# Performance work log

Hardware: AMD Instinct MI355X
Metric: run time of the kernel (lower is better)

## Reference

```python
import jax, jax.numpy as jnp
import numpy as np

WINDOW = (2, 7, 7)
NUM_HEADS = 8


def _relative_position_index(ws):
    d, h, w = ws
    coords = np.stack(np.meshgrid(np.arange(d), np.arange(h), np.arange(w), indexing='ij'), 0)
    cf = coords.reshape(3, -1)                      # [3, N]
    rel = (cf[:, :, None] - cf[:, None, :]).transpose(1, 2, 0)  # [N, N, 3]
    rel[..., 0] += d - 1
    rel[..., 1] += h - 1
    rel[..., 2] += w - 1
    idx = rel[..., 0] * ((2 * h - 1) * (2 * w - 1)) + rel[..., 1] * (2 * w - 1) + rel[..., 2]
    return idx.astype(np.int32)                     # [N, N]

_REL_IDX = _relative_position_index(WINDOW)


def setup_inputs() -> dict:
    key = jax.random.key(0)
    ks = jax.random.split(key, 6)
    B_, N, C = 2048, 98, 256
    nW = 64
    table_size = (2 * WINDOW[0] - 1) * (2 * WINDOW[1] - 1) * (2 * WINDOW[2] - 1)  # 507
    return {
        'x': jax.random.normal(ks[0], (B_, N, C), jnp.float32),
        'mask': jax.random.normal(ks[1], (nW, N, N), jnp.float32),
        'qkv_w': jax.random.normal(ks[2], (C, 3 * C), jnp.float32) * 0.02,
        'proj_w': jax.random.normal(ks[3], (C, C), jnp.float32) * 0.02,
        'proj_b': jax.random.normal(ks[4], (C,), jnp.float32) * 0.02,
        'bias_table': jax.random.normal(ks[5], (table_size, NUM_HEADS), jnp.float32) * 0.02,
    }


def reference(x, mask, qkv_w, proj_w, proj_b, bias_table):
    B_, N, C = x.shape
    H = NUM_HEADS
    Dh = C // H
    scale = Dh ** (-0.5)

    qkv = jnp.einsum('bnc,cd->bnd', x, qkv_w)               # [B_, N, 3C]
    qkv = qkv.reshape(B_, N, 3, H, Dh).transpose(2, 0, 3, 1, 4)  # [3, B_, H, N, Dh]
    q, k, v = qkv[0], qkv[1], qkv[2]

    attn = jnp.einsum('bhnd,bhmd->bhnm', q * scale, k)      # [B_, H, N, N]

    rel_idx = jnp.asarray(_REL_IDX[:N, :N])
    bias = bias_table[rel_idx.reshape(-1)].reshape(N, N, H).transpose(2, 0, 1)  # [H, N, N]
    attn = attn + bias[None]

    nW = mask.shape[0]
    attn = attn.reshape(B_ // nW, nW, H, N, N) + mask[None, :, None, :, :]
    attn = attn.reshape(B_, H, N, N)
    attn = jax.nn.softmax(attn, axis=-1)

    out = jnp.einsum('bhnm,bhmd->bhnd', attn, v)            # [B_, H, N, Dh]
    out = out.transpose(0, 2, 1, 3).reshape(B_, N, C)
    out = jnp.einsum('bnc,cd->bnd', out, proj_w) + proj_b
    return out
```

## Files before the change

### kernel.cpp

```cpp
#include <hip/hip_runtime.h>
#include <stdint.h>

typedef __bf16 bf16_t;
typedef __bf16 bf16x8 __attribute__((ext_vector_type(8)));
typedef float f32x4 __attribute__((ext_vector_type(4)));

#define MFMA16(a, b, c) __builtin_amdgcn_mfma_f32_16x16x32_bf16(a, b, c, 0, 0, 0)

__device__ __forceinline__ void gload_lds16(const bf16_t* g, bf16_t* l) {
  __builtin_amdgcn_global_load_lds(
      (const __attribute__((address_space(1))) void*)g,
      (__attribute__((address_space(3))) void*)l, 16, 0, 0);
}

__device__ __forceinline__ int sw4(int i) {
  return ((i & 3) << 2) | ((i >> 2) & 3);
}

__global__ __launch_bounds__(256) void cvt_x_k(const float* __restrict__ x,
                                               bf16_t* __restrict__ xb, int n8) {
  int i = blockIdx.x * 256 + threadIdx.x;
  if (i >= n8) return;
  const float4* xp = (const float4*)x + (size_t)i * 2;
  float4 f0 = xp[0], f1 = xp[1];
  bf16x8 o = {(bf16_t)f0.x, (bf16_t)f0.y, (bf16_t)f0.z, (bf16_t)f0.w,
              (bf16_t)f1.x, (bf16_t)f1.y, (bf16_t)f1.z, (bf16_t)f1.w};
  *(bf16x8*)(xb + (size_t)i * 8) = o;
}

__global__ __launch_bounds__(256) void cvt_wT_k(const float* __restrict__ w,
                                                bf16_t* __restrict__ wT, int N) {
  int n = blockIdx.x, k = threadIdx.x;
  wT[(size_t)n * 256 + k] = (bf16_t)w[(size_t)k * N + n];
}

__global__ __launch_bounds__(256) void gemm256(const bf16_t* __restrict__ A,
                                               const bf16_t* __restrict__ BT,
                                               int ncols,
                                               bf16_t* __restrict__ outb,
                                               float* __restrict__ outf,
                                               const float* __restrict__ bias) {
  __shared__ __align__(16) bf16_t sA[128 * 64];
  __shared__ __align__(16) bf16_t sB[128 * 64];
  const int tid = threadIdx.x;
  const int lane = tid & 63, wave = tid >> 6;
  const int lm = lane & 15, quad = lane >> 4;
  const int mBase = blockIdx.y * 128;
  const int nBase = blockIdx.x * 128;
  const int wm = (wave >> 1) * 64, wn = (wave & 1) * 64;

  f32x4 acc[4][4];
#pragma unroll
  for (int i = 0; i < 4; i++)
#pragma unroll
    for (int j = 0; j < 4; j++) acc[i][j] = {0.f, 0.f, 0.f, 0.f};

  const bf16_t* Ab = A + (size_t)mBase * 256;
  const bf16_t* Bb = BT + (size_t)nBase * 256;

  for (int kb = 0; kb < 4; ++kb) {
    const int k0 = kb * 64;
#pragma unroll
    for (int it = 0; it < 4; ++it) {
      int cid = it * 256 + wave * 64 + lane;
      int row = cid >> 3, kcp = cid & 7;
      int kcl = kcp ^ (row & 7);
      bf16_t* dstA = sA + (it * 256 + wave * 64) * 8;
      bf16_t* dstB = sB + (it * 256 + wave * 64) * 8;
      gload_lds16(Ab + (size_t)row * 256 + k0 + kcl * 8, dstA);
      gload_lds16(Bb + (size_t)row * 256 + k0 + kcl * 8, dstB);
    }
    __syncthreads();
#pragma unroll
    for (int kk = 0; kk < 64; kk += 32) {
      int c = (kk >> 3) + quad;
      bf16x8 af[4], bfr[4];
#pragma unroll
      for (int mt = 0; mt < 4; mt++) {
        int m = wm + mt * 16 + lm;
        af[mt] = *(const bf16x8*)(sA + m * 64 + ((c ^ (m & 7)) << 3));
      }
#pragma unroll
      for (int nt = 0; nt < 4; nt++) {
        int n = wn + nt * 16 + lm;
        bfr[nt] = *(const bf16x8*)(sB + n * 64 + ((c ^ (n & 7)) << 3));
      }
#pragma unroll
      for (int mt = 0; mt < 4; mt++)
#pragma unroll
        for (int nt = 0; nt < 4; nt++)
          acc[mt][nt] = MFMA16(af[mt], bfr[nt], acc[mt][nt]);
    }
    __syncthreads();
  }

  if (outb) {
#pragma unroll
    for (int mt = 0; mt < 4; mt++)
#pragma unroll
      for (int nt = 0; nt < 4; nt++) {
        int col = nBase + wn + nt * 16 + lm;
        int rbase = mBase + wm + mt * 16 + quad * 4;
#pragma unroll
        for (int r = 0; r < 4; r++)
          outb[(size_t)(rbase + r) * ncols + col] = (bf16_t)acc[mt][nt][r];
      }
  } else {
#pragma unroll
    for (int mt = 0; mt < 4; mt++)
#pragma unroll
      for (int nt = 0; nt < 4; nt++) {
        int col = nBase + wn + nt * 16 + lm;
        float bv = bias[col];
        int rbase = mBase + wm + mt * 16 + quad * 4;
#pragma unroll
        for (int r = 0; r < 4; r++)
          outf[(size_t)(rbase + r) * ncols + col] = acc[mt][nt][r] + bv;
      }
  }
}

__global__ __launch_bounds__(256, 4) void attn_win(
    const bf16_t* __restrict__ qkv, const float* __restrict__ mask,
    const float* __restrict__ btab, bf16_t* __restrict__ y) {
  __shared__ __align__(16) bf16_t sP[112 * 128];
  __shared__ __align__(16) bf16_t sVT[32 * 128];
  __shared__ float sTab[512];
  __shared__ int sU[112];

  const int tid = threadIdx.x;
  const int h = blockIdx.x, b = blockIdx.y;
  const int lane = tid & 63, wave = tid >> 6;
  const int lm = lane & 15, quad = lane >> 4;

  {
    uint4 z = {0, 0, 0, 0};
    uint4* p = (uint4*)sP;
    for (int i = tid; i < 112 * 128 / 8; i += 256) p[i] = z;
  }
  for (int idx = tid; idx < 1024; idx += 256) {
    int d = idx >> 5, j = 96 + (idx & 31);
    if (j >= 98)
      sVT[d * 128 + (((j >> 3) ^ sw4(d & 15)) << 3) + (j & 7)] = (bf16_t)0.f;
  }
  for (int i = tid; i < 507; i += 256) sTab[i] = btab[i * 8 + h];
  if (tid < 112) {
    int n = tid;
    int d = n / 49, r = n - d * 49;
    int hh = r / 7, w = r - hh * 7;
    sU[tid] = (n < 98) ? (d * 169 + hh * 13 + w) : 0;
  }

  const bf16_t* qb = qkv + (size_t)b * 98 * 768 + h * 32;

  {
    int j = tid & 127, hf = tid >> 7;
    if (j < 98) {
#pragma unroll
      for (int t = 0; t < 2; t++) {
        int dc = hf + 2 * t;
        bf16x8 v8 = *(const bf16x8*)(qb + (size_t)j * 768 + 512 + dc * 8);
#pragma unroll
        for (int e = 0; e < 8; e++) {
          int d = dc * 8 + e;
          sVT[d * 128 + (((j >> 3) ^ sw4(d & 15)) << 3) + (j & 7)] = v8[e];
        }
      }
    }
  }
  __syncthreads();

  bf16x8 kf[7];
#pragma unroll
  for (int ct = 0; ct < 7; ct++)
    kf[ct] =
        *(const bf16x8*)(qb + (size_t)(ct * 16 + lm) * 768 + 256 + quad * 8);

  f32x4 s4[2][7];
#pragma unroll
  for (int rti = 0; rti < 2; rti++) {
    int rt = wave + rti * 4;
    if (rt <= 6) {
      bf16x8 qf = *(const bf16x8*)(qb + (size_t)(rt * 16 + lm) * 768 + quad * 8);
#pragma unroll
      for (int ct = 0; ct < 7; ct++) {
        f32x4 z = {0.f, 0.f, 0.f, 0.f};
        s4[rti][ct] = MFMA16(qf, kf[ct], z);
      }
    }
  }

  const float* mp = mask + (size_t)(b & 63) * 9604;
  const float scale = 0.17677669529663687f;
  float inv[2][4];

#pragma unroll
  for (int rti = 0; rti < 2; rti++) {
    int rt = wave + rti * 4;
    if (rt > 6) continue;
    int ib = rt * 16 + quad * 4;
    int ui[4], rb[4];
#pragma unroll
    for (int r = 0; r < 4; r++) {
      int i = ib + r;
      ui[r] = sU[i] + 253;
      rb[r] = (i < 98 ? i : 97) * 98;
    }
#pragma unroll
    for (int ct = 0; ct < 7; ct++) {
      int j = ct * 16 + lm;
      int uj = sU[j];
      int jc = j < 98 ? j : 97;
      bool jv = j < 98;
#pragma unroll
      for (int r = 0; r < 4; r++) {
        float v = s4[rti][ct][r] * scale + sTab[ui[r] - uj] + mp[rb[r] + jc];
        s4[rti][ct][r] = jv ? v : -1e30f;
      }
    }
#pragma unroll
    for (int r = 0; r < 4; r++) {
      float mx = s4[rti][0][r];
#pragma unroll
      for (int ct = 1; ct < 7; ct++) mx = fmaxf(mx, s4[rti][ct][r]);
#pragma unroll
      for (int o = 1; o < 16; o <<= 1) mx = fmaxf(mx, __shfl_xor(mx, o));
      float sum = 0.f;
#pragma unroll
      for (int ct = 0; ct < 7; ct++) {
        float e = __expf(s4[rti][ct][r] - mx);
        s4[rti][ct][r] = e;
        sum += e;
      }
#pragma unroll
      for (int o = 1; o < 16; o <<= 1) sum += __shfl_xor(sum, o);
      inv[rti][r] = 1.f / sum;
    }
#pragma unroll
    for (int ct = 0; ct < 7; ct++) {
      int c2 = 2 * ct + (lm >> 3);
      int j7 = lm & 7;
#pragma unroll
      for (int r = 0; r < 4; r++) {
        int i = ib + r;
        sP[i * 128 + ((c2 ^ (4 * r + quad)) << 3) + j7] =
            (bf16_t)s4[rti][ct][r];
      }
    }
  }
  __syncthreads();

  bf16x8 vf[2][4];
#pragma unroll
  for (int dt = 0; dt < 2; dt++)
#pragma unroll
    for (int kk = 0; kk < 4; kk++) {
      int d = dt * 16 + lm;
      vf[dt][kk] =
          *(const bf16x8*)(sVT + d * 128 + (((4 * kk + quad) ^ sw4(lm)) << 3));
    }
  bf16_t* yb = y + (size_t)b * 98 * 256 + h * 32;
#pragma unroll
  for (int rti = 0; rti < 2; rti++) {
    int rt = wave + rti * 4;
    if (rt > 6) continue;
    bf16x8 af[4];
#pragma unroll
    for (int kk = 0; kk < 4; kk++) {
      int i = rt * 16 + lm;
      af[kk] =
          *(const bf16x8*)(sP + i * 128 + (((4 * kk + quad) ^ sw4(lm)) << 3));
    }
#pragma unroll
    for (int dt = 0; dt < 2; dt++) {
      f32x4 o = {0.f, 0.f, 0.f, 0.f};
#pragma unroll
      for (int kk = 0; kk < 4; kk++) o = MFMA16(af[kk], vf[dt][kk], o);
#pragma unroll
      for (int r = 0; r < 4; r++) {
        int i = rt * 16 + quad * 4 + r;
        if (i < 98)
          yb[(size_t)i * 256 + dt * 16 + lm] = (bf16_t)(o[r] * inv[rti][r]);
      }
    }
  }
}

extern "C" void kernel_launch(void* const* d_in, const int* in_sizes, int n_in,
                              void* d_out, int out_size, void* d_ws,
                              size_t ws_size, hipStream_t stream) {
  const float* x = (const float*)d_in[0];
  const float* mask = (const float*)d_in[1];
  const float* qkv_w = (const float*)d_in[2];
  const float* proj_w = (const float*)d_in[3];
  const float* proj_b = (const float*)d_in[4];
  const float* btab = (const float*)d_in[5];
  float* out = (float*)d_out;

  char* ws = (char*)d_ws;
  bf16_t* qkv = (bf16_t*)ws;
  bf16_t* ybuf = (bf16_t*)(ws + 308281344);
  bf16_t* xb = ybuf;
  bf16_t* wT = (bf16_t*)(ws + 308281344 + 102760448);
  bf16_t* pT = (bf16_t*)(ws + 308281344 + 102760448 + 393216);

  cvt_x_k<<<25088, 256, 0, stream>>>(x, xb, 6422528);
  cvt_wT_k<<<768, 256, 0, stream>>>(qkv_w, wT, 768);
  cvt_wT_k<<<256, 256, 0, stream>>>(proj_w, pT, 256);

  gemm256<<<dim3(6, 1568), 256, 0, stream>>>(xb, wT, 768, qkv, nullptr,
                                             nullptr);

  attn_win<<<dim3(8, 2048), 256, 0, stream>>>(qkv, mask, btab, ybuf);

  gemm256<<<dim3(2, 1568), 256, 0, stream>>>(ybuf, pT, 256, nullptr, out,
                                             proj_b);
}
```

Measured before the change: 804.5 us.

## Use nontemporal loads/stores and XCD-aware block remapping in GEMM

Replaces ordinary global loads and stores in the conversion, GEMM epilogue and attention kernels with nontemporal variants, so streamed data does not pollute the caches. It also remaps GEMM workgroup indices so that consecutive tiles are grouped per XCD, which is meant to improve L2 reuse of shared A/B tiles on the chiplet layout. The risk is that nontemporal hints on data that is reused (qkv rows read by several heads, the intermediate buffers read by the next kernel) could raise memory traffic instead of lowering it.

```diff
diff --git a/kernel.cpp b/kernel.cpp
--- a/kernel.cpp
+++ b/kernel.cpp
@@ -4,6 +4,7 @@
 typedef __bf16 bf16_t;
 typedef __bf16 bf16x8 __attribute__((ext_vector_type(8)));
 typedef float f32x4 __attribute__((ext_vector_type(4)));
+typedef float f32x4v __attribute__((ext_vector_type(4)));
 
 #define MFMA16(a, b, c) __builtin_amdgcn_mfma_f32_16x16x32_bf16(a, b, c, 0, 0, 0)
 
@@ -21,11 +22,12 @@
                                                bf16_t* __restrict__ xb, int n8) {
   int i = blockIdx.x * 256 + threadIdx.x;
   if (i >= n8) return;
-  const float4* xp = (const float4*)x + (size_t)i * 2;
-  float4 f0 = xp[0], f1 = xp[1];
+  const f32x4v* xp = (const f32x4v*)x + (size_t)i * 2;
+  f32x4v f0 = __builtin_nontemporal_load(xp);
+  f32x4v f1 = __builtin_nontemporal_load(xp + 1);
   bf16x8 o = {(bf16_t)f0.x, (bf16_t)f0.y, (bf16_t)f0.z, (bf16_t)f0.w,
               (bf16_t)f1.x, (bf16_t)f1.y, (bf16_t)f1.z, (bf16_t)f1.w};
-  *(bf16x8*)(xb + (size_t)i * 8) = o;
+  __builtin_nontemporal_store(o, (bf16x8*)(xb + (size_t)i * 8));
 }
 
 __global__ __launch_bounds__(256) void cvt_wT_k(const float* __restrict__ w,
@@ -45,8 +47,17 @@
   const int tid = threadIdx.x;
   const int lane = tid & 63, wave = tid >> 6;
   const int lm = lane & 15, quad = lane >> 4;
-  const int mBase = blockIdx.y * 128;
-  const int nBase = blockIdx.x * 128;
+
+  int nwg = gridDim.x * gridDim.y;
+  int L = blockIdx.y * gridDim.x + blockIdx.x;
+  if ((nwg & 7) == 0) {
+    int cpx = nwg >> 3;
+    L = (L & 7) * cpx + (L >> 3);
+  }
+  const int bx = L % gridDim.x, by = L / gridDim.x;
+
+  const int mBase = by * 128;
+  const int nBase = bx * 128;
   const int wm = (wave >> 1) * 64, wn = (wave & 1) * 64;
 
   f32x4 acc[4][4];
@@ -103,7 +114,9 @@
         int rbase = mBase + wm + mt * 16 + quad * 4;
 #pragma unroll
         for (int r = 0; r < 4; r++)
-          outb[(size_t)(rbase + r) * ncols + col] = (bf16_t)acc[mt][nt][r];
+          __builtin_nontemporal_store(
+              (bf16_t)acc[mt][nt][r],
+              outb + (size_t)(rbase + r) * ncols + col);
       }
   } else {
 #pragma unroll
@@ -115,7 +128,9 @@
         int rbase = mBase + wm + mt * 16 + quad * 4;
 #pragma unroll
         for (int r = 0; r < 4; r++)
-          outf[(size_t)(rbase + r) * ncols + col] = acc[mt][nt][r] + bv;
+          __builtin_nontemporal_store(
+              acc[mt][nt][r] + bv,
+              outf + (size_t)(rbase + r) * ncols + col);
       }
   }
 }
@@ -159,7 +174,8 @@
 #pragma unroll
       for (int t = 0; t < 2; t++) {
         int dc = hf + 2 * t;
-        bf16x8 v8 = *(const bf16x8*)(qb + (size_t)j * 768 + 512 + dc * 8);
+        bf16x8 v8 = __builtin_nontemporal_load(
+            (const bf16x8*)(qb + (size_t)j * 768 + 512 + dc * 8));
 #pragma unroll
         for (int e = 0; e < 8; e++) {
           int d = dc * 8 + e;
@@ -173,15 +189,16 @@
   bf16x8 kf[7];
 #pragma unroll
   for (int ct = 0; ct < 7; ct++)
-    kf[ct] =
-        *(const bf16x8*)(qb + (size_t)(ct * 16 + lm) * 768 + 256 + quad * 8);
+    kf[ct] = __builtin_nontemporal_load(
+        (const bf16x8*)(qb + (size_t)(ct * 16 + lm) * 768 + 256 + quad * 8));
 
   f32x4 s4[2][7];
 #pragma unroll
   for (int rti = 0; rti < 2; rti++) {
     int rt = wave + rti * 4;
     if (rt <= 6) {
-      bf16x8 qf = *(const bf16x8*)(qb + (size_t)(rt * 16 + lm) * 768 + quad * 8);
+      bf16x8 qf = __builtin_nontemporal_load(
+          (const bf16x8*)(qb + (size_t)(rt * 16 + lm) * 768 + quad * 8));
 #pragma unroll
       for (int ct = 0; ct < 7; ct++) {
         f32x4 z = {0.f, 0.f, 0.f, 0.f};
@@ -280,7 +297,9 @@
       for (int r = 0; r < 4; r++) {
         int i = rt * 16 + quad * 4 + r;
         if (i < 98)
-          yb[(size_t)i * 256 + dt * 16 + lm] = (bf16_t)(o[r] * inv[rti][r]);
+          __builtin_nontemporal_store(
+              (bf16_t)(o[r] * inv[rti][r]),
+              yb + (size_t)i * 256 + dt * 16 + lm);
       }
     }
   }
```

Measured after the change: 939.8 us. +16.8%, slower.

## Process two heads per attention block and remap GEMM workgroups across XCDs

Applied to the files above, without the earlier changes.

The attention kernel now runs 512 threads per block, covering two heads, with duplicated LDS buffers for P, V-transpose and the bias table. This halves the block count and shares the mask reads and setup between two heads. The GEMM kernel remaps its linear block index so consecutive tiles land on the same XCD (an 8-way interleave), aiming for better L2 locality. The cost is doubled LDS per block, which may reduce occupancy, and launch_bounds(512,4) puts more pressure on registers.

```diff
diff --git a/kernel.cpp b/kernel.cpp
--- a/kernel.cpp
+++ b/kernel.cpp
@@ -45,8 +45,17 @@
   const int tid = threadIdx.x;
   const int lane = tid & 63, wave = tid >> 6;
   const int lm = lane & 15, quad = lane >> 4;
-  const int mBase = blockIdx.y * 128;
-  const int nBase = blockIdx.x * 128;
+
+  int nwg = gridDim.x * gridDim.y;
+  int L = blockIdx.y * gridDim.x + blockIdx.x;
+  if ((nwg & 7) == 0) {
+    int cpx = nwg >> 3;
+    L = (L & 7) * cpx + (L >> 3);
+  }
+  const int bx = L % gridDim.x, by = L / gridDim.x;
+
+  const int mBase = by * 128;
+  const int nBase = bx * 128;
   const int wm = (wave >> 1) * 64, wn = (wave & 1) * 64;
 
   f32x4 acc[4][4];
@@ -120,30 +129,36 @@
   }
 }
 
-__global__ __launch_bounds__(256, 4) void attn_win(
+__global__ __launch_bounds__(512, 4) void attn_win(
     const bf16_t* __restrict__ qkv, const float* __restrict__ mask,
     const float* __restrict__ btab, bf16_t* __restrict__ y) {
-  __shared__ __align__(16) bf16_t sP[112 * 128];
-  __shared__ __align__(16) bf16_t sVT[32 * 128];
-  __shared__ float sTab[512];
+  __shared__ __align__(16) bf16_t sP[2][112 * 128];
+  __shared__ __align__(16) bf16_t sVT[2][32 * 128];
+  __shared__ float sTab[2][512];
   __shared__ int sU[112];
 
   const int tid = threadIdx.x;
-  const int h = blockIdx.x, b = blockIdx.y;
+  const int p = blockIdx.x, b = blockIdx.y;
   const int lane = tid & 63, wave = tid >> 6;
+  const int w4 = wave & 3, hg = wave >> 2;
+  const int h = 2 * p + hg;
   const int lm = lane & 15, quad = lane >> 4;
 
   {
     uint4 z = {0, 0, 0, 0};
-    uint4* p = (uint4*)sP;
-    for (int i = tid; i < 112 * 128 / 8; i += 256) p[i] = z;
-  }
-  for (int idx = tid; idx < 1024; idx += 256) {
-    int d = idx >> 5, j = 96 + (idx & 31);
+    uint4* pp = (uint4*)&sP[0][0];
+    for (int i = tid; i < 2 * 112 * 128 / 8; i += 512) pp[i] = z;
+  }
+  for (int idx = tid; idx < 2048; idx += 512) {
+    int g = idx >> 10, r = idx & 1023;
+    int d = r >> 5, j = 96 + (r & 31);
     if (j >= 98)
-      sVT[d * 128 + (((j >> 3) ^ sw4(d & 15)) << 3) + (j & 7)] = (bf16_t)0.f;
-  }
-  for (int i = tid; i < 507; i += 256) sTab[i] = btab[i * 8 + h];
+      sVT[g][d * 128 + (((j >> 3) ^ sw4(d & 15)) << 3) + (j & 7)] = (bf16_t)0.f;
+  }
+  for (int idx = tid; idx < 1024; idx += 512) {
+    int g = idx >> 9, i = idx & 511;
+    if (i < 507) sTab[g][i] = btab[i * 8 + 2 * p + g];
+  }
   if (tid < 112) {
     int n = tid;
     int d = n / 49, r = n - d * 49;
@@ -151,19 +166,20 @@
     sU[tid] = (n < 98) ? (d * 169 + hh * 13 + w) : 0;
   }
 
-  const bf16_t* qb = qkv + (size_t)b * 98 * 768 + h * 32;
+  const bf16_t* qh = qkv + (size_t)b * 98 * 768 + h * 32;
 
   {
-    int j = tid & 127, hf = tid >> 7;
+    int j = tid & 127, q2 = (tid >> 7) & 1, g = tid >> 8;
+    const bf16_t* qv = qkv + (size_t)b * 98 * 768 + (2 * p + g) * 32;
     if (j < 98) {
 #pragma unroll
       for (int t = 0; t < 2; t++) {
-        int dc = hf + 2 * t;
-        bf16x8 v8 = *(const bf16x8*)(qb + (size_t)j * 768 + 512 + dc * 8);
+        int dc = q2 + 2 * t;
+        bf16x8 v8 = *(const bf16x8*)(qv + (size_t)j * 768 + 512 + dc * 8);
 #pragma unroll
         for (int e = 0; e < 8; e++) {
           int d = dc * 8 + e;
-          sVT[d * 128 + (((j >> 3) ^ sw4(d & 15)) << 3) + (j & 7)] = v8[e];
+          sVT[g][d * 128 + (((j >> 3) ^ sw4(d & 15)) << 3) + (j & 7)] = v8[e];
         }
       }
     }
@@ -174,14 +190,14 @@
 #pragma unroll
   for (int ct = 0; ct < 7; ct++)
     kf[ct] =
-        *(const bf16x8*)(qb + (size_t)(ct * 16 + lm) * 768 + 256 + quad * 8);
+        *(const bf16x8*)(qh + (size_t)(ct * 16 + lm) * 768 + 256 + quad * 8);
 
   f32x4 s4[2][7];
 #pragma unroll
   for (int rti = 0; rti < 2; rti++) {
-    int rt = wave + rti * 4;
+    int rt = w4 + rti * 4;
     if (rt <= 6) {
-      bf16x8 qf = *(const bf16x8*)(qb + (size_t)(rt * 16 + lm) * 768 + quad * 8);
+      bf16x8 qf = *(const bf16x8*)(qh + (size_t)(rt * 16 + lm) * 768 + quad * 8);
 #pragma unroll
       for (int ct = 0; ct < 7; ct++) {
         f32x4 z = {0.f, 0.f, 0.f, 0.f};
@@ -196,7 +212,7 @@
 
 #pragma unroll
   for (int rti = 0; rti < 2; rti++) {
-    int rt = wave + rti * 4;
+    int rt = w4 + rti * 4;
     if (rt > 6) continue;
     int ib = rt * 16 + quad * 4;
     int ui[4], rb[4];
@@ -214,7 +230,7 @@
       bool jv = j < 98;
 #pragma unroll
       for (int r = 0; r < 4; r++) {
-        float v = s4[rti][ct][r] * scale + sTab[ui[r] - uj] + mp[rb[r] + jc];
+        float v = s4[rti][ct][r] * scale + sTab[hg][ui[r] - uj] + mp[rb[r] + jc];
         s4[rti][ct][r] = jv ? v : -1e30f;
       }
     }
@@ -243,7 +259,7 @@
 #pragma unroll
       for (int r = 0; r < 4; r++) {
         int i = ib + r;
-        sP[i * 128 + ((c2 ^ (4 * r + quad)) << 3) + j7] =
+        sP[hg][i * 128 + ((c2 ^ (4 * r + quad)) << 3) + j7] =
             (bf16_t)s4[rti][ct][r];
       }
     }
@@ -256,20 +272,20 @@
 #pragma unroll
     for (int kk = 0; kk < 4; kk++) {
       int d = dt * 16 + lm;
-      vf[dt][kk] =
-          *(const bf16x8*)(sVT + d * 128 + (((4 * kk + quad) ^ sw4(lm)) << 3));
+      vf[dt][kk] = *(const bf16x8*)(sVT[hg] + d * 128 +
+                                    (((4 * kk + quad) ^ sw4(lm)) << 3));
     }
   bf16_t* yb = y + (size_t)b * 98 * 256 + h * 32;
 #pragma unroll
   for (int rti = 0; rti < 2; rti++) {
-    int rt = wave + rti * 4;
+    int rt = w4 + rti * 4;
     if (rt > 6) continue;
     bf16x8 af[4];
 #pragma unroll
     for (int kk = 0; kk < 4; kk++) {
       int i = rt * 16 + lm;
-      af[kk] =
-          *(const bf16x8*)(sP + i * 128 + (((4 * kk + quad) ^ sw4(lm)) << 3));
+      af[kk] = *(const bf16x8*)(sP[hg] + i * 128 +
+                                (((4 * kk + quad) ^ sw4(lm)) << 3));
     }
 #pragma unroll
     for (int dt = 0; dt < 2; dt++) {
@@ -311,7 +327,7 @@
   gemm256<<<dim3(6, 1568), 256, 0, stream>>>(xb, wT, 768, qkv, nullptr,
                                              nullptr);
 
-  attn_win<<<dim3(8, 2048), 256, 0, stream>>>(qkv, mask, btab, ybuf);
+  attn_win<<<dim3(4, 2048), 512, 0, stream>>>(qkv, mask, btab, ybuf);
 
   gemm256<<<dim3(2, 1568), 256, 0, stream>>>(ybuf, pT, 256, nullptr, out,
                                              proj_b);
```

After: 863.1 us. 1.07x slower.

## Fuse x fp32-to-bf16 conversion into QKV GEMM and remap blocks for XCD locality

Applied to the files above, without the earlier changes.

The QKV GEMM now reads fp32 x directly, converts it to bf16 in registers and stores it into the swizzled LDS tile. This removes the separate conversion kernel and its round trip of a bf16 copy through global memory. The two weight-transpose kernels are merged into a single launch. GEMM and attention blocks are remapped so that neighbouring tiles or heads of the same window land on the same XCD, aiming at better L2 reuse. The trade-off is that the A tile is now loaded through registers rather than the direct global-to-LDS path, which adds VGPR pressure and latency.

```diff
diff --git a/kernel.cpp b/kernel.cpp
--- a/kernel.cpp
+++ b/kernel.cpp
@@ -17,36 +17,42 @@
   return ((i & 3) << 2) | ((i >> 2) & 3);
 }
 
-__global__ __launch_bounds__(256) void cvt_x_k(const float* __restrict__ x,
-                                               bf16_t* __restrict__ xb, int n8) {
-  int i = blockIdx.x * 256 + threadIdx.x;
-  if (i >= n8) return;
-  const float4* xp = (const float4*)x + (size_t)i * 2;
-  float4 f0 = xp[0], f1 = xp[1];
-  bf16x8 o = {(bf16_t)f0.x, (bf16_t)f0.y, (bf16_t)f0.z, (bf16_t)f0.w,
-              (bf16_t)f1.x, (bf16_t)f1.y, (bf16_t)f1.z, (bf16_t)f1.w};
-  *(bf16x8*)(xb + (size_t)i * 8) = o;
-}
-
-__global__ __launch_bounds__(256) void cvt_wT_k(const float* __restrict__ w,
-                                                bf16_t* __restrict__ wT, int N) {
-  int n = blockIdx.x, k = threadIdx.x;
-  wT[(size_t)n * 256 + k] = (bf16_t)w[(size_t)k * N + n];
-}
-
-__global__ __launch_bounds__(256) void gemm256(const bf16_t* __restrict__ A,
-                                               const bf16_t* __restrict__ BT,
-                                               int ncols,
-                                               bf16_t* __restrict__ outb,
-                                               float* __restrict__ outf,
-                                               const float* __restrict__ bias) {
+__global__ __launch_bounds__(256) void cvt_w2_k(const float* __restrict__ w1,
+                                                bf16_t* __restrict__ o1,
+                                                const float* __restrict__ w2,
+                                                bf16_t* __restrict__ o2) {
+  int blk = blockIdx.x, k = threadIdx.x;
+  if (blk < 768) {
+    o1[(size_t)blk * 256 + k] = (bf16_t)w1[(size_t)k * 768 + blk];
+  } else {
+    int n = blk - 768;
+    o2[(size_t)n * 256 + k] = (bf16_t)w2[(size_t)k * 256 + n];
+  }
+}
+
+template <bool AF32>
+__global__ __launch_bounds__(256) void gemm256_t(const void* __restrict__ Av,
+                                                 const bf16_t* __restrict__ BT,
+                                                 int ncols,
+                                                 bf16_t* __restrict__ outb,
+                                                 float* __restrict__ outf,
+                                                 const float* __restrict__ bias) {
   __shared__ __align__(16) bf16_t sA[128 * 64];
   __shared__ __align__(16) bf16_t sB[128 * 64];
   const int tid = threadIdx.x;
   const int lane = tid & 63, wave = tid >> 6;
   const int lm = lane & 15, quad = lane >> 4;
-  const int mBase = blockIdx.y * 128;
-  const int nBase = blockIdx.x * 128;
+
+  int nwg = gridDim.x * gridDim.y;
+  int L = blockIdx.y * gridDim.x + blockIdx.x;
+  if ((nwg & 7) == 0) {
+    int cpx = nwg >> 3;
+    L = (L & 7) * cpx + (L >> 3);
+  }
+  const int bx = L % gridDim.x, by = L / gridDim.x;
+
+  const int mBase = by * 128;
+  const int nBase = bx * 128;
   const int wm = (wave >> 1) * 64, wn = (wave & 1) * 64;
 
   f32x4 acc[4][4];
@@ -55,20 +61,46 @@
 #pragma unroll
     for (int j = 0; j < 4; j++) acc[i][j] = {0.f, 0.f, 0.f, 0.f};
 
-  const bf16_t* Ab = A + (size_t)mBase * 256;
+  const bf16_t* Ab = AF32 ? nullptr : (const bf16_t*)Av + (size_t)mBase * 256;
+  const float* Af = AF32 ? (const float*)Av + (size_t)mBase * 256 : nullptr;
   const bf16_t* Bb = BT + (size_t)nBase * 256;
 
   for (int kb = 0; kb < 4; ++kb) {
     const int k0 = kb * 64;
-#pragma unroll
-    for (int it = 0; it < 4; ++it) {
-      int cid = it * 256 + wave * 64 + lane;
-      int row = cid >> 3, kcp = cid & 7;
-      int kcl = kcp ^ (row & 7);
-      bf16_t* dstA = sA + (it * 256 + wave * 64) * 8;
-      bf16_t* dstB = sB + (it * 256 + wave * 64) * 8;
-      gload_lds16(Ab + (size_t)row * 256 + k0 + kcl * 8, dstA);
-      gload_lds16(Bb + (size_t)row * 256 + k0 + kcl * 8, dstB);
+    if constexpr (AF32) {
+      f32x4 fa[4][2];
+#pragma unroll
+      for (int it = 0; it < 4; ++it) {
+        int cid = it * 256 + wave * 64 + lane;
+        int row = cid >> 3, kcp = cid & 7;
+        int kcl = kcp ^ (row & 7);
+        const f32x4* src = (const f32x4*)(Af + (size_t)row * 256 + k0 + kcl * 8);
+        fa[it][0] = src[0];
+        fa[it][1] = src[1];
+      }
+#pragma unroll
+      for (int it = 0; it < 4; ++it) {
+        int cid = it * 256 + wave * 64 + lane;
+        int row = cid >> 3, kcp = cid & 7;
+        bf16_t* dstB = sB + (it * 256 + wave * 64) * 8;
+        gload_lds16(Bb + (size_t)row * 256 + k0 + (kcp ^ (row & 7)) * 8, dstB);
+        bf16x8 o = {(bf16_t)fa[it][0][0], (bf16_t)fa[it][0][1],
+                    (bf16_t)fa[it][0][2], (bf16_t)fa[it][0][3],
+                    (bf16_t)fa[it][1][0], (bf16_t)fa[it][1][1],
+                    (bf16_t)fa[it][1][2], (bf16_t)fa[it][1][3]};
+        *(bf16x8*)(sA + (size_t)cid * 8) = o;
+      }
+    } else {
+#pragma unroll
+      for (int it = 0; it < 4; ++it) {
+        int cid = it * 256 + wave * 64 + lane;
+        int row = cid >> 3, kcp = cid & 7;
+        int kcl = kcp ^ (row & 7);
+        bf16_t* dstA = sA + (it * 256 + wave * 64) * 8;
+        bf16_t* dstB = sB + (it * 256 + wave * 64) * 8;
+        gload_lds16(Ab + (size_t)row * 256 + k0 + kcl * 8, dstA);
+        gload_lds16(Bb + (size_t)row * 256 + k0 + kcl * 8, dstB);
+      }
     }
     __syncthreads();
 #pragma unroll
@@ -129,7 +161,12 @@
   __shared__ int sU[112];
 
   const int tid = threadIdx.x;
-  const int h = blockIdx.x, b = blockIdx.y;
+  const int L = blockIdx.x;
+  const int qd = L >> 4, rr = L & 15;
+  const int g = rr >> 3, x = rr & 7;
+  const int bidx = qd * 8 + x;
+  const int b = bidx >> 2;
+  const int h = ((bidx & 3) << 1) | g;
   const int lane = tid & 63, wave = tid >> 6;
   const int lm = lane & 15, quad = lane >> 4;
 
@@ -300,19 +337,16 @@
   char* ws = (char*)d_ws;
   bf16_t* qkv = (bf16_t*)ws;
   bf16_t* ybuf = (bf16_t*)(ws + 308281344);
-  bf16_t* xb = ybuf;
   bf16_t* wT = (bf16_t*)(ws + 308281344 + 102760448);
   bf16_t* pT = (bf16_t*)(ws + 308281344 + 102760448 + 393216);
 
-  cvt_x_k<<<25088, 256, 0, stream>>>(x, xb, 6422528);
-  cvt_wT_k<<<768, 256, 0, stream>>>(qkv_w, wT, 768);
-  cvt_wT_k<<<256, 256, 0, stream>>>(proj_w, pT, 256);
-
-  gemm256<<<dim3(6, 1568), 256, 0, stream>>>(xb, wT, 768, qkv, nullptr,
-                                             nullptr);
-
-  attn_win<<<dim3(8, 2048), 256, 0, stream>>>(qkv, mask, btab, ybuf);
-
-  gemm256<<<dim3(2, 1568), 256, 0, stream>>>(ybuf, pT, 256, nullptr, out,
-                                             proj_b);
-}
+  cvt_w2_k<<<1024, 256, 0, stream>>>(qkv_w, wT, proj_w, pT);
+
+  gemm256_t<true><<<dim3(6, 1568), 256, 0, stream>>>(x, wT, 768, qkv, nullptr,
+                                                     nullptr);
+
+  attn_win<<<16384, 256, 0, stream>>>(qkv, mask, btab, ybuf);
+
+  gemm256_t<false><<<dim3(2, 1568), 256, 0, stream>>>(ybuf, pT, 256, nullptr,
+                                                      out, proj_b);
+}
```

Measured after the change: 729.1 us. 9.4% less time.
